# Kernel optimization log

Measured on AMD Instinct MI355X. Metric: run time of the kernel, lower is better.

The kernel has to match this reference:

```python
import jax, jax.numpy as jnp
import numpy as np

IRE = 1.0 / 400.0

def _stencil(f):
    # f: [B, C, X, Y]; returns (u,v) 5-point stencil fields, each [B, X-2, Y-2]
    m = f[:, :, 1:-1, 1:-1]
    l = f[:, :, :-2, 1:-1]
    r = f[:, :, 2:, 1:-1]
    b = f[:, :, 1:-1, :-2]
    t = f[:, :, 1:-1, 2:]
    return (m[:, 0], m[:, 1], l[:, 0], l[:, 1], r[:, 0], r[:, 1],
            b[:, 0], b[:, 1], t[:, 0], t[:, 1])

def _residuals(um, vm, ul, vl, ur, vr, ub, vb, ut, vt):
    dudx = (ur - ul) * 0.5
    dvdy = (vt - vb) * 0.5
    dudy = (ut - ub) * 0.5
    dvdx = (vr - vl) * 0.5
    du2dx = 0.25 * ((ur + um) ** 2 - (ul + um) ** 2)
    duvdy = 0.25 * ((ut + um) * (vt + vm) - (ub + um) * (vb + vm))
    dv2dy = 0.25 * ((vt + vm) ** 2 - (vb + vm) ** 2)
    dvudx = 0.25 * ((vr + vm) * (ur + um) - (vl + vm) * (ul + um))
    dudx2 = ur - um * 2 + ul
    dudy2 = ut - um * 2 + ub
    dvdx2 = vr - vm * 2 + vl
    dvdy2 = vt - vm * 2 + vb
    mass = dudx + dvdy
    mom_u = du2dx + duvdy - (dudx2 + dudy2) * IRE
    mom_v = dvudx + dv2dy - (dvdx2 + dvdy2) * IRE
    return mass, mom_u, mom_v, dudx, dudy, dvdx, dvdy

def setup_inputs() -> dict:
    key = jax.random.key(0)
    k1, k2 = jax.random.split(key)
    pred = jax.random.normal(k1, (64, 2, 512, 512), dtype=jnp.float32)
    trut = jax.random.normal(k2, (64, 2, 512, 512), dtype=jnp.float32)
    return {"pred": pred, "trut": trut}

def reference(pred, trut):
    mass_t, momu_t, momv_t, dudx_t, dudy_t, dvdx_t, dvdy_t = _residuals(*_stencil(trut))
    mass_p, momu_p, momv_p, dudx_p, dudy_p, dvdx_p, dvdy_p = _residuals(*_stencil(pred))
    lossMass = jnp.mean(jnp.abs(mass_t - mass_p))
    lossMom = jnp.mean(jnp.abs(momu_t - momu_p) + jnp.abs(momv_t - momv_p))
    lossGdl = jnp.mean(jnp.abs(dudx_t - dudx_p) + jnp.abs(dudy_t - dudy_p)
                       + jnp.abs(dvdx_t - dvdx_p) + jnp.abs(dvdy_t - dvdy_p)) / 4.0
    lossL1 = jnp.mean(jnp.abs(pred - trut))
    # lossGdl computed (as in original) but unused in the final combination
    del lossGdl
    return (lossMass * 5 + lossMom * 25 + lossL1) / 3
```

## Files before the change

### kernel.cpp

```cpp
#include <hip/hip_runtime.h>

#define IRE (1.0f / 400.0f)

constexpr int W  = 512;
constexpr int H  = 512;
constexpr int NB = 64;
constexpr int TR = 32;
constexpr int TILES = H / TR;
constexpr int NBLK  = NB * TILES;
constexpr int NSLOT = 5;


__device__ __forceinline__ void residuals3(
    float um, float vm, float ul, float vl, float ur, float vr,
    float ub, float vb, float ut, float vt,
    float& mass, float& momu, float& momv)
{
    float dudx = (ur - ul) * 0.5f;
    float dvdy = (vt - vb) * 0.5f;
    float ru = ur + um, lu = ul + um, tu_ = ut + um, bu = ub + um;
    float rv = vr + vm, lv = vl + vm, tv_ = vt + vm, bv = vb + vm;
    float du2dx = 0.25f * (ru * ru - lu * lu);
    float duvdy = 0.25f * (tu_ * tv_ - bu * bv);
    float dv2dy = 0.25f * (tv_ * tv_ - bv * bv);
    float dvudx = 0.25f * (rv * ru - lv * lu);
    float dudx2 = ur - 2.0f * um + ul;
    float dudy2 = ut - 2.0f * um + ub;
    float dvdx2 = vr - 2.0f * vm + vl;
    float dvdy2 = vt - 2.0f * vm + vb;
    mass = dudx + dvdy;
    momu = du2dx + duvdy - (dudx2 + dudy2) * IRE;
    momv = dvudx + dv2dy - (dvdx2 + dvdy2) * IRE;
}

struct W8 { float c0, c1, lf, rt, u0, u1, d0, d1; };

__global__ __launch_bounds__(256, 4) void loss_main(
    const float* __restrict__ pred, const float* __restrict__ trut,
    double* __restrict__ partial)
{
    __shared__ __align__(16) float ring[NSLOT * 4 * W];

    const int tid  = (int)threadIdx.x;
    const int lane = tid & 63;
    const int wv   = tid >> 6;
    const int blk  = (int)blockIdx.x;
    const int tile = blk % TILES;
    const int b    = blk / TILES;
    const int r0   = tile * TR;

    const size_t CH = (size_t)H * W;
    const float* gbase = (wv < 2 ? trut : pred) + (size_t)b * 2 * CH + (size_t)(wv & 1) * CH;

    auto stage_row = [&](int row, int slot) {
        row = row < 0 ? 0 : (row > H - 1 ? H - 1 : row);
        const float* src = gbase + (size_t)row * W + lane * 4;
        float* dst = &ring[(slot * 4 + wv) * W];
        __builtin_amdgcn_global_load_lds(
            (const __attribute__((address_space(1))) void*)src,
            (__attribute__((address_space(3))) void*)dst, 16, 0, 0);
        __builtin_amdgcn_global_load_lds(
            (const __attribute__((address_space(1))) void*)(src + 256),
            (__attribute__((address_space(3))) void*)(dst + 256), 16, 0, 0);
    };

    stage_row(r0 - 1, 0);
    stage_row(r0,     1);
    stage_row(r0 + 1, 2);

    const int j0  = tid * 2;
    const int jm1 = (j0 == 0) ? 0 : j0 - 1;
    const int jp2 = (j0 + 2 > W - 1) ? W - 1 : j0 + 2;

    float accMass = 0.0f, accMom = 0.0f, accL1 = 0.0f;

    int sTop = 0;
    for (int s = 0; s < TR; ++s) {
        const int r = r0 + s;
        if (s < TR - 1) {
            int sSt = sTop + 3; if (sSt >= NSLOT) sSt -= NSLOT;
            stage_row(r + 2, sSt);
            asm volatile("s_waitcnt vmcnt(2) lgkmcnt(0)\n\ts_barrier" ::: "memory");
        } else {
            asm volatile("s_waitcnt vmcnt(0) lgkmcnt(0)\n\ts_barrier" ::: "memory");
        }

        int sMid = sTop + 1; if (sMid >= NSLOT) sMid -= NSLOT;
        int sBot = sMid + 1; if (sBot >= NSLOT) sBot -= NSLOT;
        const float* top = &ring[sTop * 4 * W];
        const float* mid = &ring[sMid * 4 * W];
        const float* bot = &ring[sBot * 4 * W];

        W8 wtu, wtv, wpu, wpv;
        #define LOADA(dst, a) \
            dst.c0 = mid[(a)*W + j0]; dst.c1 = mid[(a)*W + j0 + 1]; \
            dst.lf = mid[(a)*W + jm1]; dst.rt = mid[(a)*W + jp2]; \
            dst.u0 = top[(a)*W + j0]; dst.u1 = top[(a)*W + j0 + 1]; \
            dst.d0 = bot[(a)*W + j0]; dst.d1 = bot[(a)*W + j0 + 1];
        LOADA(wtu, 0) LOADA(wtv, 1) LOADA(wpu, 2) LOADA(wpv, 3)
        #undef LOADA

        accL1 += fabsf(wpu.c0 - wtu.c0) + fabsf(wpu.c1 - wtu.c1)
               + fabsf(wpv.c0 - wtv.c0) + fabsf(wpv.c1 - wtv.c1);

        if (r >= 1 && r <= H - 2) {
            float mT, uT, vT, mP, uP, vP;
            residuals3(wtu.c0, wtv.c0, wtu.u0, wtv.u0, wtu.d0, wtv.d0,
                       wtu.lf, wtv.lf, wtu.c1, wtv.c1, mT, uT, vT);
            residuals3(wpu.c0, wpv.c0, wpu.u0, wpv.u0, wpu.d0, wpv.d0,
                       wpu.lf, wpv.lf, wpu.c1, wpv.c1, mP, uP, vP);
            if (j0 >= 1) {
                accMass += fabsf(mT - mP);
                accMom  += fabsf(uT - uP) + fabsf(vT - vP);
            }
            residuals3(wtu.c1, wtv.c1, wtu.u1, wtv.u1, wtu.d1, wtv.d1,
                       wtu.c0, wtv.c0, wtu.rt, wtv.rt, mT, uT, vT);
            residuals3(wpu.c1, wpv.c1, wpu.u1, wpv.u1, wpu.d1, wpv.d1,
                       wpu.c0, wpv.c0, wpu.rt, wpv.rt, mP, uP, vP);
            if (j0 + 1 <= W - 2) {
                accMass += fabsf(mT - mP);
                accMom  += fabsf(uT - uP) + fabsf(vT - vP);
            }
        }
        sTop = sMid;
    }

    float res = 5.0f * accMass + 25.0f * accMom;
    float l1  = accL1;
    #pragma unroll
    for (int off = 32; off > 0; off >>= 1) {
        res += __shfl_down(res, off);
        l1  += __shfl_down(l1, off);
    }
    __syncthreads();
    double* sred = (double*)ring;
    if (lane == 0) { sred[wv] = (double)res; sred[4 + wv] = (double)l1; }
    __syncthreads();
    if (tid == 0) {
        partial[(size_t)blk * 2 + 0] = sred[0] + sred[1] + sred[2] + sred[3];
        partial[(size_t)blk * 2 + 1] = sred[4] + sred[5] + sred[6] + sred[7];
    }
}

__global__ __launch_bounds__(256) void loss_final(
    const double* __restrict__ partial, float* __restrict__ out)
{
    __shared__ double sres[4], sl1[4];
    const int t = (int)threadIdx.x;
    double res = 0.0, l1 = 0.0;
    for (int i = t; i < NBLK; i += 256) {
        res += partial[(size_t)i * 2 + 0];
        l1  += partial[(size_t)i * 2 + 1];
    }
    #pragma unroll
    for (int off = 32; off > 0; off >>= 1) {
        res += __shfl_down(res, off);
        l1  += __shfl_down(l1, off);
    }
    const int wave = t >> 6;
    if ((t & 63) == 0) { sres[wave] = res; sl1[wave] = l1; }
    __syncthreads();
    if (t == 0) {
        res = sres[0] + sres[1] + sres[2] + sres[3];
        l1  = sl1[0] + sl1[1] + sl1[2] + sl1[3];
        const double nRes = 64.0 * 510.0 * 510.0;
        const double nL1  = 64.0 * 2.0 * 512.0 * 512.0;
        out[0] = (float)((res / nRes + l1 / nL1) / 3.0);
    }
}

extern "C" void kernel_launch(void* const* d_in, const int* in_sizes, int n_in,
                              void* d_out, int out_size, void* d_ws, size_t ws_size,
                              hipStream_t stream)
{
    const float* pred = (const float*)d_in[0];
    const float* trut = (const float*)d_in[1];
    double* partial = (double*)d_ws;
    loss_main<<<NBLK, 256, 0, stream>>>(pred, trut, partial);
    loss_final<<<1, 256, 0, stream>>>(partial, (float*)d_out);
}
```

Baseline: 288.7 us.

## Keep stencil rows in registers and shrink LDS ring to four slots

Stencil rows now slide through registers: each step reads only the new bottom row from LDS, using float2 loads for the centre pair, and shifts top/mid/bot in registers. The ring buffer drops from five slots to four with power-of-two slot indexing, and the row loop is unrolled by four. This cuts LDS read traffic per row by about two thirds and lowers shared memory per block, which may allow more blocks per CU. It costs more live registers per thread and leaves less slack in the ring for overwriting a slot that is still being read.

```diff
diff --git a/kernel.cpp b/kernel.cpp
--- a/kernel.cpp
+++ b/kernel.cpp
@@ -8,7 +8,7 @@
 constexpr int TR = 32;
 constexpr int TILES = H / TR;
 constexpr int NBLK  = NB * TILES;
-constexpr int NSLOT = 5;
+constexpr int NSLOT = 4;
 
 
 __device__ __forceinline__ void residuals3(
@@ -33,8 +33,6 @@
     momv = dvudx + dv2dy - (dvdx2 + dvdy2) * IRE;
 }
 
-struct W8 { float c0, c1, lf, rt, u0, u1, d0, d1; };
-
 __global__ __launch_bounds__(256, 4) void loss_main(
     const float* __restrict__ pred, const float* __restrict__ trut,
     double* __restrict__ partial)
@@ -55,7 +53,7 @@
     auto stage_row = [&](int row, int slot) {
         row = row < 0 ? 0 : (row > H - 1 ? H - 1 : row);
         const float* src = gbase + (size_t)row * W + lane * 4;
-        float* dst = &ring[(slot * 4 + wv) * W];
+        float* dst = &ring[slot * (4 * W) + wv * W];
         __builtin_amdgcn_global_load_lds(
             (const __attribute__((address_space(1))) void*)src,
             (__attribute__((address_space(3))) void*)dst, 16, 0, 0);
@@ -74,55 +72,68 @@
 
     float accMass = 0.0f, accMom = 0.0f, accL1 = 0.0f;
 
-    int sTop = 0;
+    float2 topc[4], midc[4], botc[4];
+    float  midl[4], midr[4], botl[4], botr[4];
+
+    asm volatile("s_waitcnt vmcnt(2)\n\ts_barrier" ::: "memory");
+    #pragma unroll
+    for (int a = 0; a < 4; ++a) {
+        const float* p0 = &ring[0 * (4 * W) + a * W];
+        const float* p1 = &ring[1 * (4 * W) + a * W];
+        topc[a] = *(const float2*)(p0 + j0);
+        midc[a] = *(const float2*)(p1 + j0);
+        midl[a] = p1[jm1];
+        midr[a] = p1[jp2];
+    }
+
+    #pragma unroll 4
     for (int s = 0; s < TR; ++s) {
         const int r = r0 + s;
         if (s < TR - 1) {
-            int sSt = sTop + 3; if (sSt >= NSLOT) sSt -= NSLOT;
-            stage_row(r + 2, sSt);
+            stage_row(r + 2, (s + 3) & 3);
             asm volatile("s_waitcnt vmcnt(2) lgkmcnt(0)\n\ts_barrier" ::: "memory");
         } else {
             asm volatile("s_waitcnt vmcnt(0) lgkmcnt(0)\n\ts_barrier" ::: "memory");
         }
 
-        int sMid = sTop + 1; if (sMid >= NSLOT) sMid -= NSLOT;
-        int sBot = sMid + 1; if (sBot >= NSLOT) sBot -= NSLOT;
-        const float* top = &ring[sTop * 4 * W];
-        const float* mid = &ring[sMid * 4 * W];
-        const float* bot = &ring[sBot * 4 * W];
+        const float* bp = &ring[((s + 2) & 3) * (4 * W)];
+        #pragma unroll
+        for (int a = 0; a < 4; ++a) {
+            botc[a] = *(const float2*)(bp + a * W + j0);
+            botl[a] = bp[a * W + jm1];
+            botr[a] = bp[a * W + jp2];
+        }
 
-        W8 wtu, wtv, wpu, wpv;
-        #define LOADA(dst, a) \
-            dst.c0 = mid[(a)*W + j0]; dst.c1 = mid[(a)*W + j0 + 1]; \
-            dst.lf = mid[(a)*W + jm1]; dst.rt = mid[(a)*W + jp2]; \
-            dst.u0 = top[(a)*W + j0]; dst.u1 = top[(a)*W + j0 + 1]; \
-            dst.d0 = bot[(a)*W + j0]; dst.d1 = bot[(a)*W + j0 + 1];
-        LOADA(wtu, 0) LOADA(wtv, 1) LOADA(wpu, 2) LOADA(wpv, 3)
-        #undef LOADA
-
-        accL1 += fabsf(wpu.c0 - wtu.c0) + fabsf(wpu.c1 - wtu.c1)
-               + fabsf(wpv.c0 - wtv.c0) + fabsf(wpv.c1 - wtv.c1);
+        accL1 += fabsf(midc[2].x - midc[0].x) + fabsf(midc[2].y - midc[0].y)
+               + fabsf(midc[3].x - midc[1].x) + fabsf(midc[3].y - midc[1].y);
 
         if (r >= 1 && r <= H - 2) {
             float mT, uT, vT, mP, uP, vP;
-            residuals3(wtu.c0, wtv.c0, wtu.u0, wtv.u0, wtu.d0, wtv.d0,
-                       wtu.lf, wtv.lf, wtu.c1, wtv.c1, mT, uT, vT);
-            residuals3(wpu.c0, wpv.c0, wpu.u0, wpv.u0, wpu.d0, wpv.d0,
-                       wpu.lf, wpv.lf, wpu.c1, wpv.c1, mP, uP, vP);
+            residuals3(midc[0].x, midc[1].x, topc[0].x, topc[1].x, botc[0].x, botc[1].x,
+                       midl[0],   midl[1],   midc[0].y, midc[1].y, mT, uT, vT);
+            residuals3(midc[2].x, midc[3].x, topc[2].x, topc[3].x, botc[2].x, botc[3].x,
+                       midl[2],   midl[3],   midc[2].y, midc[3].y, mP, uP, vP);
             if (j0 >= 1) {
                 accMass += fabsf(mT - mP);
                 accMom  += fabsf(uT - uP) + fabsf(vT - vP);
             }
-            residuals3(wtu.c1, wtv.c1, wtu.u1, wtv.u1, wtu.d1, wtv.d1,
-                       wtu.c0, wtv.c0, wtu.rt, wtv.rt, mT, uT, vT);
-            residuals3(wpu.c1, wpv.c1, wpu.u1, wpv.u1, wpu.d1, wpv.d1,
-                       wpu.c0, wpv.c0, wpu.rt, wpv.rt, mP, uP, vP);
+            residuals3(midc[0].y, midc[1].y, topc[0].y, topc[1].y, botc[0].y, botc[1].y,
+                       midc[0].x, midc[1].x, midr[0],   midr[1],   mT, uT, vT);
+            residuals3(midc[2].y, midc[3].y, topc[2].y, topc[3].y, botc[2].y, botc[3].y,
+                       midc[2].x, midc[3].x, midr[2],   midr[3],   mP, uP, vP);
             if (j0 + 1 <= W - 2) {
                 accMass += fabsf(mT - mP);
                 accMom  += fabsf(uT - uP) + fabsf(vT - vP);
             }
         }
-        sTop = sMid;
+
+        #pragma unroll
+        for (int a = 0; a < 4; ++a) {
+            topc[a] = midc[a];
+            midc[a] = botc[a];
+            midl[a] = botl[a];
+            midr[a] = botr[a];
+        }
     }
 
     float res = 5.0f * accMass + 25.0f * accMom;
```

Measured after the change: 284.2 us. Within noise of the previous version (-1.6%).
